# Optimization experiments

Hardware: AMD Instinct MI355X
Metric: run time of the kernel (lower is better)

The kernel has to match this reference:

```python
import jax, jax.numpy as jnp
import numpy as np

NUM = 128
IN_F = NUM * NUM        # 16384
HID = NUM * 3           # 384 (infl_ratio = 3)
OUT = 10
BATCH = 8192
BN_EPS = 1e-5


def sign_ste(t):
    # Deterministic sign binarization with straight-through gradient,
    # matching the torch .data/.org mutation trick.
    return t + jax.lax.stop_gradient(jnp.sign(t) - t)


def setup_inputs() -> dict:
    key = jax.random.key(0)
    k_x, k_w1, k_w4 = jax.random.split(key, 3)
    x = jax.random.normal(k_x, (BATCH, IN_F), dtype=jnp.float32)
    W1 = jax.random.normal(k_w1, (HID, IN_F), dtype=jnp.float32) * 0.02
    W4 = jax.random.normal(k_w4, (OUT, HID), dtype=jnp.float32) * 0.02
    gamma = jnp.ones((HID,), dtype=jnp.float32)
    beta = jnp.zeros((HID,), dtype=jnp.float32)
    return {"x": x, "W1": W1, "gamma": gamma, "beta": beta, "W4": W4}


def reference(x, W1, gamma, beta, W4):
    x = x.reshape(-1, IN_F)
    # fc1: in_features (16384) != 784, so the hard-coded check binarizes the input too
    xb = sign_ste(x)
    h = jnp.einsum('bk,hk->bh', xb, sign_ste(W1))  # [B, HID]
    # BatchNorm1d, training mode: batch stats, biased variance
    mean = jnp.mean(h, axis=0)
    var = jnp.mean(jnp.square(h - mean), axis=0)
    h = (h - mean) * jax.lax.rsqrt(var + BN_EPS) * gamma + beta
    # Hardtanh
    h = jnp.clip(h, -1.0, 1.0)
    # fc4: input size 384 != 784 -> binarize activations, binarize weights
    out = jnp.einsum('bh,oh->bo', sign_ste(h), sign_ste(W4))  # [B, 10]
    return out
```

## Files before the change

### kernel.cpp

```cpp
#include <hip/hip_runtime.h>
#include <cstdint>
#include <cstddef>


typedef float v4f __attribute__((ext_vector_type(4)));

#define BATCH   8192
#define KDIM    16384
#define HID     384
#define OUT_F   10
#define BK      64
#define MT      32
#define NITER   (KDIM / BK)
#define CHUNK_B (HID * BK)

#define WS_W1C   0
#define WS_H     (6291456)
#define WS_GSUM  (WS_H + 12582912)
#define WS_GSQ   (WS_GSUM + 3072)
#define WS_MEAN  (WS_GSQ + 3072)
#define WS_COEF  (WS_MEAN + 3072)
#define WS_SW4   (WS_COEF + 3072)

__device__ __forceinline__ uint32_t pack_sign4(v4f v) {
    uint32_t p = 0;
#pragma unroll
    for (int i = 0; i < 4; ++i) {
        uint32_t u = __float_as_uint(v[i]);
        uint32_t b = ((u & 0x7fffffffu) == 0u) ? 0u : (0x38u | ((u >> 24) & 0x80u));
        p |= b << (8 * i);
    }
    return p;
}

__global__ void prep_w1(const float* __restrict__ W1, uint8_t* __restrict__ W1c) {
    size_t e = ((size_t)blockIdx.x * blockDim.x + threadIdx.x) * 4;
    int n = (int)(e / KDIM);
    int k = (int)(e & (KDIM - 1));
    v4f w = *(const v4f*)(W1 + e);
    uint32_t p = pack_sign4(w);
    int chunk = k >> 6;
    int kin = k & 63;
    int gx = (kin >> 3) ^ (n & 7);
    *(uint32_t*)(W1c + (size_t)chunk * CHUNK_B + n * 64 + gx * 8 + (kin & 7)) = p;
}

__device__ __forceinline__ void gll16(const void* g, void* l) {
    __builtin_amdgcn_global_load_lds(
        (__attribute__((address_space(1))) void*)(void*)(g),
        (__attribute__((address_space(3))) void*)(l),
        16, 0, 0);
}

__global__ __launch_bounds__(512, 2) void gemm1(const float* __restrict__ x,
                                                const uint8_t* __restrict__ W1c,
                                                float* __restrict__ h) {
    __shared__ __align__(16) uint8_t Ws[2][CHUNK_B];
    __shared__ __align__(16) uint8_t Xs[2][MT * 72];

    const int t    = threadIdx.x;
    const int wave = t >> 6;
    const int lane = t & 63;
    const int q    = lane >> 4;
    const int l15  = lane & 15;
    const int m0   = blockIdx.x * MT;

    const int xrow = t >> 4;
    const int xk4  = (t & 15) * 4;
    const float* xp = x + (size_t)(m0 + xrow) * KDIM + xk4;

    v4f acc[2][3];
#pragma unroll
    for (int mt = 0; mt < 2; ++mt)
#pragma unroll
        for (int nt = 0; nt < 3; ++nt)
            acc[mt][nt] = v4f{0.f, 0.f, 0.f, 0.f};

    {
        const uint8_t* src = W1c + (size_t)wave * 3072 + (size_t)lane * 16;
#pragma unroll
        for (int r = 0; r < 3; ++r)
            gll16(src + r * 1024, &Ws[0][wave * 3072 + r * 1024]);
        v4f xv = *(const v4f*)(xp);
        *(uint32_t*)&Xs[0][xrow * 72 + xk4] = pack_sign4(xv);
    }
    __syncthreads();

#pragma unroll 2
    for (int it = 0; it < NITER; ++it) {
        const int cur = it & 1;
        const int nxt = cur ^ 1;
        const bool more = (it + 1) < NITER;
        v4f xv;
        if (more) {
            const uint8_t* src = W1c + (size_t)(it + 1) * CHUNK_B
                               + (size_t)wave * 3072 + (size_t)lane * 16;
#pragma unroll
            for (int r = 0; r < 3; ++r)
                gll16(src + r * 1024, &Ws[nxt][wave * 3072 + r * 1024]);
            xv = *(const v4f*)(xp + (size_t)(it + 1) * BK);
        }

#pragma unroll
        for (int s = 0; s < 2; ++s) {
            long long a[2], b[3];
#pragma unroll
            for (int mt = 0; mt < 2; ++mt) {
                int m = mt * 16 + l15;
                a[mt] = *(const long long*)&Xs[cur][m * 72 + s * 32 + q * 8];
            }
#pragma unroll
            for (int nt = 0; nt < 3; ++nt) {
                int n = wave * 48 + nt * 16 + l15;
                int g = (s * 4 + q) ^ (n & 7);
                b[nt] = *(const long long*)&Ws[cur][n * 64 + g * 8];
            }
#pragma unroll
            for (int mt = 0; mt < 2; ++mt)
#pragma unroll
                for (int nt = 0; nt < 3; ++nt)
                    acc[mt][nt] = __builtin_amdgcn_mfma_f32_16x16x32_fp8_fp8(
                        a[mt], b[nt], acc[mt][nt], 0, 0, 0);
        }

        if (more) {
            *(uint32_t*)&Xs[nxt][xrow * 72 + xk4] = pack_sign4(xv);
        }
        __syncthreads();
    }

#pragma unroll
    for (int mt = 0; mt < 2; ++mt)
#pragma unroll
        for (int nt = 0; nt < 3; ++nt)
#pragma unroll
            for (int r = 0; r < 4; ++r) {
                int row = m0 + mt * 16 + q * 4 + r;
                int col = wave * 48 + nt * 16 + l15;
                h[(size_t)row * HID + col] = acc[mt][nt][r];
            }
}

__global__ void colstats(const float* __restrict__ h,
                         double* __restrict__ gsum, double* __restrict__ gsq) {
    int j  = threadIdx.x;
    int r0 = blockIdx.x * 128;
    double s = 0.0, sq = 0.0;
    for (int r = 0; r < 128; ++r) {
        double v = (double)h[(size_t)(r0 + r) * HID + j];
        s += v;
        sq += v * v;
    }
    atomicAdd(&gsum[j], s);
    atomicAdd(&gsq[j], sq);
}

__global__ void finalize(const double* __restrict__ gsum, const double* __restrict__ gsq,
                         const float* __restrict__ gamma, const float* __restrict__ W4,
                         double* __restrict__ meanArr, double* __restrict__ coefArr,
                         float* __restrict__ sW4) {
    int j = threadIdx.x;
    double mean = gsum[j] * (1.0 / (double)BATCH);
    double var  = gsq[j] * (1.0 / (double)BATCH) - mean * mean;
    meanArr[j] = mean;
    coefArr[j] = (double)gamma[j] / sqrt(var + 1e-5);
#pragma unroll
    for (int o = 0; o < OUT_F; ++o) {
        float w = W4[o * HID + j];
        sW4[o * HID + j] = (w > 0.f) ? 1.f : ((w < 0.f) ? -1.f : 0.f);
    }
}

__global__ __launch_bounds__(256) void head(const float* __restrict__ h,
                                            const double* __restrict__ meanArr,
                                            const double* __restrict__ coefArr,
                                            const float* __restrict__ beta,
                                            const float* __restrict__ sW4,
                                            float* __restrict__ out) {
    int wave = threadIdx.x >> 6;
    int lane = threadIdx.x & 63;
    int b = blockIdx.x * 4 + wave;
    float a[OUT_F];
#pragma unroll
    for (int o = 0; o < OUT_F; ++o) a[o] = 0.f;
#pragma unroll
    for (int i = 0; i < 6; ++i) {
        int j = lane + i * 64;
        double v = ((double)h[(size_t)b * HID + j] - meanArr[j]) * coefArr[j]
                 + (double)beta[j];
        float s = (v > 0.0) ? 1.f : ((v < 0.0) ? -1.f : 0.f);
#pragma unroll
        for (int o = 0; o < OUT_F; ++o) a[o] += s * sW4[o * HID + j];
    }
#pragma unroll
    for (int o = 0; o < OUT_F; ++o) {
#pragma unroll
        for (int off = 32; off > 0; off >>= 1) a[o] += __shfl_down(a[o], off);
    }
    if (lane == 0) {
#pragma unroll
        for (int o = 0; o < OUT_F; ++o) out[(size_t)b * OUT_F + o] = a[o];
    }
}

extern "C" void kernel_launch(void* const* d_in, const int* in_sizes, int n_in,
                              void* d_out, int out_size, void* d_ws, size_t ws_size,
                              hipStream_t stream) {
    const float* x     = (const float*)d_in[0];
    const float* W1    = (const float*)d_in[1];
    const float* gamma = (const float*)d_in[2];
    const float* beta  = (const float*)d_in[3];
    const float* W4    = (const float*)d_in[4];
    float* out = (float*)d_out;

    uint8_t* ws = (uint8_t*)d_ws;
    uint8_t* W1c      = ws + WS_W1C;
    float*   h        = (float*)(ws + WS_H);
    double*  gsum     = (double*)(ws + WS_GSUM);
    double*  gsq      = (double*)(ws + WS_GSQ);
    double*  meanArr  = (double*)(ws + WS_MEAN);
    double*  coefArr  = (double*)(ws + WS_COEF);
    float*   sW4      = (float*)(ws + WS_SW4);

    prep_w1<<<6144, 256, 0, stream>>>(W1, W1c);
    hipMemsetAsync(gsum, 0, 2 * HID * sizeof(double), stream);
    gemm1<<<BATCH / MT, 512, 0, stream>>>(x, W1c, h);
    colstats<<<BATCH / 128, HID, 0, stream>>>(h, gsum, gsq);
    finalize<<<1, HID, 0, stream>>>(gsum, gsq, gamma, W4, meanArr, coefArr, sW4);
    head<<<BATCH / 4, 256, 0, stream>>>(h, meanArr, coefArr, beta, sW4, out);
}
```

Baseline: 968.4 us.

## Split-K gemm1 with register-resident W1 fragments and atomic accumulation

Splits the K dimension of the binarized GEMM four ways so there are four times as many blocks. Each 4-wave block covers all 384 columns, and each lane loads its fp8 W1 fragments straight into registers, using a relaid-out W1c, instead of staging them in LDS. Partial results go into a zeroed h buffer with float atomics, and colstats uses more, smaller blocks. This trades LDS traffic and low occupancy for atomic write traffic, an extra 12MB memset, and non-deterministic summation order.

```diff
diff --git a/kernel.cpp b/kernel.cpp
--- a/kernel.cpp
+++ b/kernel.cpp
@@ -4,6 +4,7 @@
 
 
 typedef float v4f __attribute__((ext_vector_type(4)));
+typedef long long v2l __attribute__((ext_vector_type(2)));
 
 #define BATCH   8192
 #define KDIM    16384
@@ -11,8 +12,10 @@
 #define OUT_F   10
 #define BK      64
 #define MT      32
-#define NITER   (KDIM / BK)
-#define CHUNK_B (HID * BK)
+#define SPLITK  4
+#define KPB     (KDIM / SPLITK)
+#define NIT     (KPB / BK)
+#define WCHUNK  (HID * BK)
 
 #define WS_W1C   0
 #define WS_H     (6291456)
@@ -35,27 +38,21 @@
 
 __global__ void prep_w1(const float* __restrict__ W1, uint8_t* __restrict__ W1c) {
     size_t e = ((size_t)blockIdx.x * blockDim.x + threadIdx.x) * 4;
-    int n = (int)(e / KDIM);
-    int k = (int)(e & (KDIM - 1));
+    int c   = (int)(e >> 14);
+    int k   = (int)(e & 16383);
+    int it  = k >> 6;
+    int kin = k & 63;
+    int s   = kin >> 5;
+    int q   = (kin >> 3) & 3;
+    int j   = kin & 7;
     v4f w = *(const v4f*)(W1 + e);
     uint32_t p = pack_sign4(w);
-    int chunk = k >> 6;
-    int kin = k & 63;
-    int gx = (kin >> 3) ^ (n & 7);
-    *(uint32_t*)(W1c + (size_t)chunk * CHUNK_B + n * 64 + gx * 8 + (kin & 7)) = p;
-}
-
-__device__ __forceinline__ void gll16(const void* g, void* l) {
-    __builtin_amdgcn_global_load_lds(
-        (__attribute__((address_space(1))) void*)(void*)(g),
-        (__attribute__((address_space(3))) void*)(l),
-        16, 0, 0);
-}
-
-__global__ __launch_bounds__(512, 2) void gemm1(const float* __restrict__ x,
+    *(uint32_t*)(W1c + (((size_t)it * HID + c) * 4 + q) * 16 + s * 8 + j) = p;
+}
+
+__global__ __launch_bounds__(256, 4) void gemm1(const float* __restrict__ x,
                                                 const uint8_t* __restrict__ W1c,
                                                 float* __restrict__ h) {
-    __shared__ __align__(16) uint8_t Ws[2][CHUNK_B];
     __shared__ __align__(16) uint8_t Xs[2][MT * 72];
 
     const int t    = threadIdx.x;
@@ -63,90 +60,92 @@
     const int lane = t & 63;
     const int q    = lane >> 4;
     const int l15  = lane & 15;
-    const int m0   = blockIdx.x * MT;
-
-    const int xrow = t >> 4;
-    const int xk4  = (t & 15) * 4;
-    const float* xp = x + (size_t)(m0 + xrow) * KDIM + xk4;
-
-    v4f acc[2][3];
+    const int kblk = blockIdx.x & (SPLITK - 1);
+    const int m0   = (blockIdx.x >> 2) * MT;
+
+    const int xrow = t >> 3;
+    const int xk8  = (t & 7) * 8;
+    const float* xp = x + (size_t)(m0 + xrow) * KDIM + (size_t)kblk * KPB + xk8;
+
+    const uint8_t* wp = W1c + (size_t)kblk * ((size_t)NIT * WCHUNK)
+                      + (((size_t)(wave * 96 + l15)) * 4 + q) * 16;
+
+    v4f acc[2][6];
 #pragma unroll
     for (int mt = 0; mt < 2; ++mt)
 #pragma unroll
-        for (int nt = 0; nt < 3; ++nt)
+        for (int nt = 0; nt < 6; ++nt)
             acc[mt][nt] = v4f{0.f, 0.f, 0.f, 0.f};
 
+    v2l wc[6];
     {
-        const uint8_t* src = W1c + (size_t)wave * 3072 + (size_t)lane * 16;
-#pragma unroll
-        for (int r = 0; r < 3; ++r)
-            gll16(src + r * 1024, &Ws[0][wave * 3072 + r * 1024]);
-        v4f xv = *(const v4f*)(xp);
-        *(uint32_t*)&Xs[0][xrow * 72 + xk4] = pack_sign4(xv);
+#pragma unroll
+        for (int nt = 0; nt < 6; ++nt)
+            wc[nt] = *(const v2l*)(wp + nt * 1024);
+        v4f xa = *(const v4f*)(xp);
+        v4f xb = *(const v4f*)(xp + 4);
+        uint2 pk; pk.x = pack_sign4(xa); pk.y = pack_sign4(xb);
+        *(uint2*)&Xs[0][xrow * 72 + xk8] = pk;
     }
     __syncthreads();
 
 #pragma unroll 2
-    for (int it = 0; it < NITER; ++it) {
+    for (int it = 0; it < NIT; ++it) {
         const int cur = it & 1;
-        const int nxt = cur ^ 1;
-        const bool more = (it + 1) < NITER;
-        v4f xv;
+        const bool more = (it + 1) < NIT;
+        v2l wn[6];
+        v4f xa, xb;
         if (more) {
-            const uint8_t* src = W1c + (size_t)(it + 1) * CHUNK_B
-                               + (size_t)wave * 3072 + (size_t)lane * 16;
-#pragma unroll
-            for (int r = 0; r < 3; ++r)
-                gll16(src + r * 1024, &Ws[nxt][wave * 3072 + r * 1024]);
-            xv = *(const v4f*)(xp + (size_t)(it + 1) * BK);
+            const uint8_t* wpn = wp + (size_t)(it + 1) * WCHUNK;
+#pragma unroll
+            for (int nt = 0; nt < 6; ++nt)
+                wn[nt] = *(const v2l*)(wpn + nt * 1024);
+            xa = *(const v4f*)(xp + (size_t)(it + 1) * BK);
+            xb = *(const v4f*)(xp + (size_t)(it + 1) * BK + 4);
         }
 
 #pragma unroll
         for (int s = 0; s < 2; ++s) {
-            long long a[2], b[3];
-#pragma unroll
-            for (int mt = 0; mt < 2; ++mt) {
-                int m = mt * 16 + l15;
-                a[mt] = *(const long long*)&Xs[cur][m * 72 + s * 32 + q * 8];
-            }
-#pragma unroll
-            for (int nt = 0; nt < 3; ++nt) {
-                int n = wave * 48 + nt * 16 + l15;
-                int g = (s * 4 + q) ^ (n & 7);
-                b[nt] = *(const long long*)&Ws[cur][n * 64 + g * 8];
-            }
+            long long a[2];
 #pragma unroll
             for (int mt = 0; mt < 2; ++mt)
-#pragma unroll
-                for (int nt = 0; nt < 3; ++nt)
+                a[mt] = *(const long long*)&Xs[cur][(mt * 16 + l15) * 72 + s * 32 + q * 8];
+#pragma unroll
+            for (int nt = 0; nt < 6; ++nt)
+#pragma unroll
+                for (int mt = 0; mt < 2; ++mt)
                     acc[mt][nt] = __builtin_amdgcn_mfma_f32_16x16x32_fp8_fp8(
-                        a[mt], b[nt], acc[mt][nt], 0, 0, 0);
+                        a[mt], wc[nt][s], acc[mt][nt], 0, 0, 0);
         }
 
         if (more) {
-            *(uint32_t*)&Xs[nxt][xrow * 72 + xk4] = pack_sign4(xv);
+            uint2 pk; pk.x = pack_sign4(xa); pk.y = pack_sign4(xb);
+            *(uint2*)&Xs[cur ^ 1][xrow * 72 + xk8] = pk;
+#pragma unroll
+            for (int nt = 0; nt < 6; ++nt) wc[nt] = wn[nt];
         }
         __syncthreads();
     }
 
 #pragma unroll
-    for (int mt = 0; mt < 2; ++mt)
-#pragma unroll
-        for (int nt = 0; nt < 3; ++nt)
-#pragma unroll
-            for (int r = 0; r < 4; ++r) {
-                int row = m0 + mt * 16 + q * 4 + r;
-                int col = wave * 48 + nt * 16 + l15;
-                h[(size_t)row * HID + col] = acc[mt][nt][r];
-            }
+    for (int nt = 0; nt < 6; ++nt) {
+        const int col = wave * 96 + nt * 16 + l15;
+#pragma unroll
+        for (int mt = 0; mt < 2; ++mt)
+#pragma unroll
+            for (int r = 0; r < 4; ++r)
+                atomicAdd(&h[(size_t)(m0 + mt * 16 + q * 4 + r) * HID + col],
+                          acc[mt][nt][r]);
+    }
 }
 
 __global__ void colstats(const float* __restrict__ h,
                          double* __restrict__ gsum, double* __restrict__ gsq) {
     int j  = threadIdx.x;
-    int r0 = blockIdx.x * 128;
+    int r0 = blockIdx.x * 16;
     double s = 0.0, sq = 0.0;
-    for (int r = 0; r < 128; ++r) {
+#pragma unroll
+    for (int r = 0; r < 16; ++r) {
         double v = (double)h[(size_t)(r0 + r) * HID + j];
         s += v;
         sq += v * v;
@@ -214,18 +213,18 @@
     float* out = (float*)d_out;
 
     uint8_t* ws = (uint8_t*)d_ws;
-    uint8_t* W1c      = ws + WS_W1C;
-    float*   h        = (float*)(ws + WS_H);
-    double*  gsum     = (double*)(ws + WS_GSUM);
-    double*  gsq      = (double*)(ws + WS_GSQ);
-    double*  meanArr  = (double*)(ws + WS_MEAN);
-    double*  coefArr  = (double*)(ws + WS_COEF);
-    float*   sW4      = (float*)(ws + WS_SW4);
+    uint8_t* W1c     = ws + WS_W1C;
+    float*   h       = (float*)(ws + WS_H);
+    double*  gsum    = (double*)(ws + WS_GSUM);
+    double*  gsq     = (double*)(ws + WS_GSQ);
+    double*  meanArr = (double*)(ws + WS_MEAN);
+    double*  coefArr = (double*)(ws + WS_COEF);
+    float*   sW4     = (float*)(ws + WS_SW4);
 
     prep_w1<<<6144, 256, 0, stream>>>(W1, W1c);
-    hipMemsetAsync(gsum, 0, 2 * HID * sizeof(double), stream);
-    gemm1<<<BATCH / MT, 512, 0, stream>>>(x, W1c, h);
-    colstats<<<BATCH / 128, HID, 0, stream>>>(h, gsum, gsq);
+    hipMemsetAsync(ws + WS_H, 0, 12582912 + 2 * HID * sizeof(double), stream);
+    gemm1<<<(BATCH / MT) * SPLITK, 256, 0, stream>>>(x, W1c, h);
+    colstats<<<BATCH / 16, HID, 0, stream>>>(h, gsum, gsq);
     finalize<<<1, HID, 0, stream>>>(gsum, gsq, gamma, W4, meanArr, coefArr, sW4);
     head<<<BATCH / 4, 256, 0, stream>>>(h, meanArr, coefArr, beta, sW4, out);
 }
```

New measurement: 795.3 us. -17.9%, faster.
